# Kernel optimization log

Measured on AMD Instinct MI355X. Metric: run time of the kernel, lower is better.

## Reference

```python
import jax, jax.numpy as jnp
import numpy as np

BOX = 256      # box_size
OS = 1         # oversampling
NC = 10        # n_classes
B = 16         # batch
N = 262144     # points per example


def setup_inputs() -> dict:
    key = jax.random.key(0)
    k1, k2 = jax.random.split(key)
    # coordinates in [-0.5, 0.5) so (points+0.5)*S lies inside the grid
    points = jax.random.uniform(k1, (B, 2, N), dtype=jnp.float32, minval=-0.5, maxval=0.5)
    values = jax.random.normal(k2, (B, NC, N), dtype=jnp.float32)
    return {"points": points, "values": values}


def reference(points, values):
    S = BOX * OS
    b, nc = points.shape[0], values.shape[1]
    # [B,2,N] -> [B,N,2], scaled into pixel coords
    p = jnp.swapaxes((points + 0.5) * S, 1, 2)
    xyf = jnp.floor(p)
    r = p - xyf                       # fractional part, [B,N,2]
    xy = xyf.astype(jnp.int32)
    x, y = xy[..., 0], xy[..., 1]     # [B,N]
    rx, ry = r[..., 0], r[..., 1]

    im = jnp.zeros((b, nc, S * S), dtype=values.dtype)

    def scat(acc, idx, contrib):
        # acc [NC, S*S], idx [N], contrib [NC, N]
        return acc.at[:, idx].add(contrib)

    scat_b = jax.vmap(scat)  # over batch

    # 4-corner bilinear (CIC) deposition
    for dx in (0, 1):
        x_ = x + dx
        wx = (1 - dx) + (2 * dx - 1) * rx
        for dy in (0, 1):
            y_ = y + dy
            wy = (1 - dy) + (2 * dy - 1) * ry
            valid = (x_ >= 0) & (x_ < S) & (y_ >= 0) & (y_ < S)
            idx = jnp.where(valid, y_ * S + x_, 0)           # [B,N]
            w = jnp.where(valid, wx * wy, 0.0)               # [B,N]
            im = scat_b(im, idx, w[:, None, :] * values)     # [B,NC,S*S]

    return im.reshape(b, nc, S, S)
```

## Files before the change

kernel.cpp:

```cpp
#include <hip/hip_runtime.h>

#define S_     256
#define NC_    10
#define CHUNK  1024
#define TS     32
#define NBIN2  64
#define CAPR   4608
#define IW     33
#define IMSZ   (NC_ * IW * IW)
#define FPSCALE 262144.0f
#define FPINV   (1.0f / 262144.0f)

typedef unsigned int u32;

__device__ __forceinline__ u32 f2bf(float f) {
    u32 u = __float_as_uint(f);
    return (u + 0x7fffu + ((u >> 16) & 1u)) >> 16;
}
__device__ __forceinline__ float bf2f(u32 h) { return __uint_as_float(h << 16); }


__global__ void __launch_bounds__(256)
k_scatter(const float* __restrict__ points, const float* __restrict__ values,
          u32* __restrict__ cursor, u32* __restrict__ ovfCnt,
          u32* __restrict__ ovfBuf, uint2* __restrict__ recs, int N) {
    __shared__ u32 cnt[NBIN2];
    __shared__ u32 gOff[NBIN2];
    __shared__ unsigned char binId[CHUNK];
    __shared__ u32 lw[6][CHUNK];

    const int tid = threadIdx.x;
    const int cpb = N / CHUNK;
    const int b  = blockIdx.x / cpb;
    const int n0 = (blockIdx.x % cpb) * CHUNK;
    const float* pb = points + (size_t)b * 2 * N;
    const float* vb = values + (size_t)b * NC_ * N;
    const int nb = n0 + tid * 4;

    if (tid < NBIN2) cnt[tid] = 0;

    const float4 pxv = *(const float4*)(pb + nb);
    const float4 pyv = *(const float4*)(pb + (size_t)N + nb);
    float4 vv[NC_];
#pragma unroll
    for (int c = 0; c < NC_; ++c)
        vv[c] = *(const float4*)(vb + (size_t)c * N + nb);

    __syncthreads();

    float px4[4] = {pxv.x, pxv.y, pxv.z, pxv.w};
    float py4[4] = {pyv.x, pyv.y, pyv.z, pyv.w};
    u32 w0[4], binA[4];
#pragma unroll
    for (int k = 0; k < 4; ++k) {
        float px = (px4[k] + 0.5f) * (float)S_;
        float py = (py4[k] + 0.5f) * (float)S_;
        int xi = (int)floorf(px), yi = (int)floorf(py);
        u32 qx = __float2uint_rn((px - (float)(xi & ~31)) * 2048.0f);
        u32 qy = __float2uint_rn((py - (float)(yi & ~31)) * 2048.0f);
        qx = min(qx, 65535u); qy = min(qy, 65535u);
        w0[k] = qx | (qy << 16);
        binA[k] = (u32)(((yi >> 5) << 3) + (xi >> 5));
        atomicAdd(&cnt[binA[k]], 1u);
    }
    __syncthreads();

    if (tid < NBIN2) {
        u32 myCnt = cnt[tid];
        u32 x = myCnt;
#pragma unroll
        for (int off = 1; off < 64; off <<= 1) {
            u32 y = __shfl_up(x, off, 64);
            if (tid >= off) x += y;
        }
        u32 excl = x - myCnt;
        u32 gt = (u32)b * NBIN2 + (u32)tid;
        u32 gbase = 0;
        if (myCnt) gbase = gt * (u32)CAPR + atomicAdd(&cursor[gt], myCnt);
        gOff[tid] = gbase - excl;
        cnt[tid] = excl;
    }
    __syncthreads();

#pragma unroll
    for (int k = 0; k < 4; ++k) {
        u32 bin = binA[k];
        u32 slot = atomicAdd(&cnt[bin], 1u);
        binId[slot] = (unsigned char)bin;
#define VG(c) ((&vv[c].x)[k])
        lw[0][slot] = w0[k];
        lw[1][slot] = f2bf(VG(0)) | (f2bf(VG(1)) << 16);
        lw[2][slot] = f2bf(VG(2)) | (f2bf(VG(3)) << 16);
        lw[3][slot] = f2bf(VG(4)) | (f2bf(VG(5)) << 16);
        lw[4][slot] = f2bf(VG(6)) | (f2bf(VG(7)) << 16);
        lw[5][slot] = f2bf(VG(8)) | (f2bf(VG(9)) << 16);
#undef VG
    }
    __syncthreads();

    const u32 tb0 = (u32)b * NBIN2;
#pragma unroll
    for (int k = 0; k < 4; ++k) {
        u32 r = (u32)tid + (u32)k * 256;
        u32 bin = binId[r];
        u32 dst = gOff[bin] + r;
        u32 a0 = lw[0][r], a1 = lw[1][r], a2 = lw[2][r],
            a3 = lw[3][r], a4 = lw[4][r], a5 = lw[5][r];
        u32 rel = dst - (tb0 + bin) * (u32)CAPR;
        if (rel < (u32)CAPR) {
            size_t s3 = (size_t)dst * 3;
            recs[s3]     = make_uint2(a0, a1);
            recs[s3 + 1] = make_uint2(a2, a3);
            recs[s3 + 2] = make_uint2(a4, a5);
        } else {
            u32 oi = atomicAdd(ovfCnt, 1u);
            u32* ob = ovfBuf + (size_t)oi * 7;
            ob[0] = tb0 + bin;
            ob[1] = a0; ob[2] = a1; ob[3] = a2;
            ob[4] = a3; ob[5] = a4; ob[6] = a5;
        }
    }
}

__global__ void __launch_bounds__(256)
k_fused(const uint2* __restrict__ recs, const u32* __restrict__ cursor,
        float* __restrict__ out, float* __restrict__ borderBuf) {
    __shared__ u32 img[IMSZ];

    const int tid = threadIdx.x;
    const int g = blockIdx.x;
    const int batch = g >> 6, t = g & 63;
    const int ox = (t & 7) * TS, oy = (t >> 3) * TS;
    const u32 base = (u32)g * (u32)CAPR;
    const u32 n = min(cursor[g], (u32)CAPR);

    for (int p = tid; p < IMSZ; p += 256) img[p] = 0u;
    __syncthreads();

    for (u32 i = tid; i < n; i += 256) {
        size_t sa = (size_t)(base + i) * 3;
        uint2 a = recs[sa], b2 = recs[sa + 1], c2 = recs[sa + 2];
        u32 qx = a.x & 0xffffu, qy = a.x >> 16;
        int xi = (int)(qx >> 11), yi = (int)(qy >> 11);
        float rx = (float)(qx & 2047u) * (1.0f / 2048.0f);
        float ry = (float)(qy & 2047u) * (1.0f / 2048.0f);
        float w00 = (1.0f - rx) * (1.0f - ry) * FPSCALE;
        float w10 = rx * (1.0f - ry) * FPSCALE;
        float w01 = (1.0f - rx) * ry * FPSCALE;
        float w11 = rx * ry * FPSCALE;
        int p00 = yi * IW + xi;
        float v[NC_];
        v[0] = bf2f(a.y & 0xffffu);  v[1] = bf2f(a.y >> 16);
        v[2] = bf2f(b2.x & 0xffffu); v[3] = bf2f(b2.x >> 16);
        v[4] = bf2f(b2.y & 0xffffu); v[5] = bf2f(b2.y >> 16);
        v[6] = bf2f(c2.x & 0xffffu); v[7] = bf2f(c2.x >> 16);
        v[8] = bf2f(c2.y & 0xffffu); v[9] = bf2f(c2.y >> 16);
#pragma unroll
        for (int c = 0; c < NC_; ++c) {
            float vc = v[c];
            u32* ib = img + c * (IW * IW) + p00;
            atomicAdd(ib,          (u32)__float2int_rn(w00 * vc));
            atomicAdd(ib + 1,      (u32)__float2int_rn(w10 * vc));
            atomicAdd(ib + IW,     (u32)__float2int_rn(w01 * vc));
            atomicAdd(ib + IW + 1, (u32)__float2int_rn(w11 * vc));
        }
    }
    __syncthreads();

    for (int p = tid; p < IW * IW; p += 256) {
        int lx = p % IW, ly = p / IW;
        bool interior = (lx >= 1) & (lx <= 31) & (ly >= 1) & (ly <= 31);
        if (interior) {
            int gx = ox + lx, gy = oy + ly;
            float* ob = out + (size_t)batch * NC_ * S_ * S_ + gy * S_ + gx;
#pragma unroll
            for (int q = 0; q < NC_; ++q)
                ob[(size_t)q * S_ * S_] =
                    (float)(int)img[q * (IW * IW) + p] * FPINV;
        } else {
            float* bb = borderBuf + ((size_t)g * (IW * IW) + p) * NC_;
#pragma unroll
            for (int q = 0; q < NC_; ++q)
                bb[q] = (float)(int)img[q * (IW * IW) + p] * FPINV;
        }
    }
}

#define CLEAN_T 4096
__global__ void __launch_bounds__(256)
k_border(const float* __restrict__ borderBuf, float* __restrict__ out,
         const u32* __restrict__ ovfCnt, const u32* __restrict__ ovfBuf,
         int total) {
    int idx = blockIdx.x * 256 + threadIdx.x;
    if (idx >= total) {
        u32 oc = *ovfCnt;
        for (u32 j = (u32)(idx - total); j < oc; j += CLEAN_T) {
            const u32* ob = ovfBuf + (size_t)j * 7;
            u32 g = ob[0];
            int batch = (int)(g >> 6), t = (int)(g & 63u);
            int ox = (t & 7) * TS, oy = (t >> 3) * TS;
            u32 w0 = ob[1];
            u32 qx = w0 & 0xffffu, qy = w0 >> 16;
            int xi = ox + (int)(qx >> 11), yi = oy + (int)(qy >> 11);
            float rx = (float)(qx & 2047u) * (1.0f / 2048.0f);
            float ry = (float)(qy & 2047u) * (1.0f / 2048.0f);
            float v[NC_];
            v[0] = bf2f(ob[2] & 0xffffu); v[1] = bf2f(ob[2] >> 16);
            v[2] = bf2f(ob[3] & 0xffffu); v[3] = bf2f(ob[3] >> 16);
            v[4] = bf2f(ob[4] & 0xffffu); v[5] = bf2f(ob[4] >> 16);
            v[6] = bf2f(ob[5] & 0xffffu); v[7] = bf2f(ob[5] >> 16);
            v[8] = bf2f(ob[6] & 0xffffu); v[9] = bf2f(ob[6] >> 16);
            float* obase = out + (size_t)batch * NC_ * S_ * S_;
            for (int dx = 0; dx < 2; ++dx) {
                int x_ = xi + dx; if (x_ >= S_) continue;
                float wx = dx ? rx : (1.0f - rx);
                for (int dy = 0; dy < 2; ++dy) {
                    int y_ = yi + dy; if (y_ >= S_) continue;
                    float w = wx * (dy ? ry : (1.0f - ry));
                    for (int cc = 0; cc < NC_; ++cc)
                        atomicAdd(obase + (size_t)cc * S_ * S_ + y_ * S_ + x_,
                                  w * v[cc]);
                }
            }
        }
        return;
    }
    int b = idx / 4032;
    int j = idx - b * 4032;
    int gx, gy;
    if (j < 2048) {
        gx = (j >> 8) << 5;
        gy = j & 255;
    } else {
        int j2 = j - 2048;
        int row = j2 / 248, col = j2 - row * 248;
        gy = row << 5;
        gx = col + 1 + col / 31;
    }

    int txs[2], lxs[2], nx = 0;
    bool bx = (gx & 31) == 0, by = (gy & 31) == 0;
    if (bx) {
        if (gx > 0) { txs[nx] = (gx >> 5) - 1; lxs[nx] = 32; ++nx; }
        txs[nx] = gx >> 5; lxs[nx] = 0; ++nx;
    } else { txs[0] = gx >> 5; lxs[0] = gx & 31; nx = 1; }
    int tys[2], lys[2], ny = 0;
    if (by) {
        if (gy > 0) { tys[ny] = (gy >> 5) - 1; lys[ny] = 32; ++ny; }
        tys[ny] = gy >> 5; lys[ny] = 0; ++ny;
    } else { tys[0] = gy >> 5; lys[0] = gy & 31; ny = 1; }

    float acc[NC_];
#pragma unroll
    for (int q = 0; q < NC_; ++q) acc[q] = 0.0f;
    for (int jj = 0; jj < ny; ++jj)
        for (int ii = 0; ii < nx; ++ii) {
            int g = (b << 6) + (tys[jj] << 3) + txs[ii];
            int p = lys[jj] * IW + lxs[ii];
            const float* bb = borderBuf + ((size_t)g * (IW * IW) + p) * NC_;
#pragma unroll
            for (int q = 0; q < NC_; ++q) acc[q] += bb[q];
        }
    float* ob = out + (size_t)b * NC_ * S_ * S_ + gy * S_ + gx;
#pragma unroll
    for (int q = 0; q < NC_; ++q) ob[(size_t)q * S_ * S_] = acc[q];
}

__global__ void __launch_bounds__(256)
scatter_cic_kernel(const float* __restrict__ points,
                   const float* __restrict__ values,
                   float* __restrict__ out, int N) {
    const int n = blockIdx.x * blockDim.x + threadIdx.x;
    const int b = blockIdx.y;
    if (n >= N) return;
    const float* pb = points + (size_t)b * 2 * N;
    const float px = (pb[n] + 0.5f) * (float)S_;
    const float py = (pb[(size_t)N + n] + 0.5f) * (float)S_;
    const float xf = floorf(px), yf = floorf(py);
    const float rx = px - xf, ry = py - yf;
    const int xi = (int)xf, yi = (int)yf;
    const float* vb = values + (size_t)b * NC_ * N + n;
    float v[NC_];
#pragma unroll
    for (int c = 0; c < NC_; ++c) v[c] = vb[(size_t)c * N];
    float* ob = out + (size_t)b * NC_ * S_ * S_;
#pragma unroll
    for (int dx = 0; dx < 2; ++dx) {
        const int x_ = xi + dx;
        if (x_ < 0 || x_ >= S_) continue;
        const float wx = dx ? rx : (1.0f - rx);
#pragma unroll
        for (int dy = 0; dy < 2; ++dy) {
            const int y_ = yi + dy;
            if (y_ < 0 || y_ >= S_) continue;
            const float w = wx * (dy ? ry : (1.0f - ry));
            const int idx = y_ * S_ + x_;
#pragma unroll
            for (int c = 0; c < NC_; ++c)
                atomicAdd(ob + (size_t)c * S_ * S_ + idx, w * v[c]);
        }
    }
}

extern "C" void kernel_launch(void* const* d_in, const int* in_sizes, int n_in,
                              void* d_out, int out_size, void* d_ws, size_t ws_size,
                              hipStream_t stream) {
    const float* points = (const float*)d_in[0];
    const float* values = (const float*)d_in[1];
    float* out = (float*)d_out;

    const int B = out_size / (NC_ * S_ * S_);
    const int N = in_sizes[0] / (2 * B);

    const size_t P = (size_t)B * N;
    const int cpb = N / CHUNK;
    const int chunksTotal = B * cpb;
    const int nSlab = B * NBIN2;

    const size_t recBytes    = (size_t)nSlab * CAPR * 24;
    const size_t borderElems = (size_t)nSlab * (IW * IW) * NC_;
    const size_t ovfBytes    = P * 7 * 4;
    const size_t wsNeeded    = recBytes + (size_t)(nSlab + 1) * 4 +
                               borderElems * 4 + ovfBytes + 256;

    const bool fast = (N % CHUNK == 0) && (N >= CHUNK) && (B > 0) &&
                      (P < (1u << 31) / 2) && (ws_size >= wsNeeded);

    if (fast) {
        char* w = (char*)d_ws;
        uint2* recsA     = (uint2*)w;
        u32* cursor      = (u32*)(w + recBytes);
        u32* ovfCnt      = cursor + nSlab;
        float* borderBuf = (float*)(ovfCnt + 1);
        u32* ovfBuf      = (u32*)(borderBuf + borderElems);

        hipMemsetAsync(cursor, 0, (size_t)(nSlab + 1) * 4, stream);
        k_scatter<<<chunksTotal, 256, 0, stream>>>(points, values, cursor,
                                                   ovfCnt, ovfBuf, recsA, N);
        k_fused<<<nSlab, 256, 0, stream>>>(recsA, cursor, out, borderBuf);
        const int borderTotal = B * 4032;
        k_border<<<(borderTotal + 255) / 256 + CLEAN_T / 256, 256, 0, stream>>>(
            borderBuf, out, ovfCnt, ovfBuf, borderTotal);
    } else {
        hipMemsetAsync(d_out, 0, (size_t)out_size * sizeof(float), stream);
        dim3 block(256, 1, 1);
        dim3 grid((N + 255) / 256, B, 1);
        scatter_cic_kernel<<<grid, block, 0, stream>>>(points, values, out, N);
    }
}
```

Baseline: 352.4 us.

## Process two chunks per scatter block with early loads and prefetch records in fused

The scatter kernel now handles two 1024-point chunks per block. All loads for both chunks are issued up front through inline global_load_dwordx4, and explicit s_waitcnt vmcnt counts let the second chunk's loads stay in flight while the first chunk is binned and written. The fused kernel software-pipelines its record loop by loading the next record's three uint2 words before doing the atomics for the current one. This relies on hand-placed wait counts that the compiler cannot check, and it halves the scatter grid size and raises register pressure.

```diff
diff --git a/kernel.cpp b/kernel.cpp
--- a/kernel.cpp
+++ b/kernel.cpp
@@ -12,12 +12,16 @@
 #define FPINV   (1.0f / 262144.0f)
 
 typedef unsigned int u32;
+typedef float f32x4 __attribute__((ext_vector_type(4)));
 
 __device__ __forceinline__ u32 f2bf(float f) {
     u32 u = __float_as_uint(f);
     return (u + 0x7fffu + ((u >> 16) & 1u)) >> 16;
 }
 __device__ __forceinline__ float bf2f(u32 h) { return __uint_as_float(h << 16); }
+
+#define GLOAD4(dst, addr) \
+    asm volatile("global_load_dwordx4 %0, %1, off" : "=v"(dst) : "v"(addr))
 
 
 __global__ void __launch_bounds__(256)
@@ -30,96 +34,111 @@
     __shared__ u32 lw[6][CHUNK];
 
     const int tid = threadIdx.x;
-    const int cpb = N / CHUNK;
-    const int b  = blockIdx.x / cpb;
-    const int n0 = (blockIdx.x % cpb) * CHUNK;
+    const int ppb = N / (2 * CHUNK);
+    const int b  = blockIdx.x / ppb;
+    const int n0 = (blockIdx.x % ppb) * (2 * CHUNK);
     const float* pb = points + (size_t)b * 2 * N;
     const float* vb = values + (size_t)b * NC_ * N;
-    const int nb = n0 + tid * 4;
+    const int nA = n0 + tid * 4;
+    const int nB = nA + CHUNK;
+
+    f32x4 pxA, pyA, pxB, pyB, vA[NC_], vB[NC_];
+    GLOAD4(pxA, pb + nA);
+    GLOAD4(pyA, pb + (size_t)N + nA);
+    GLOAD4(pxB, pb + nB);
+    GLOAD4(pyB, pb + (size_t)N + nB);
+#pragma unroll
+    for (int c = 0; c < NC_; ++c) GLOAD4(vA[c], vb + (size_t)c * N + nA);
+#pragma unroll
+    for (int c = 0; c < NC_; ++c) GLOAD4(vB[c], vb + (size_t)c * N + nB);
 
     if (tid < NBIN2) cnt[tid] = 0;
-
-    const float4 pxv = *(const float4*)(pb + nb);
-    const float4 pyv = *(const float4*)(pb + (size_t)N + nb);
-    float4 vv[NC_];
-#pragma unroll
-    for (int c = 0; c < NC_; ++c)
-        vv[c] = *(const float4*)(vb + (size_t)c * N + nb);
-
-    __syncthreads();
-
-    float px4[4] = {pxv.x, pxv.y, pxv.z, pxv.w};
-    float py4[4] = {pyv.x, pyv.y, pyv.z, pyv.w};
-    u32 w0[4], binA[4];
-#pragma unroll
-    for (int k = 0; k < 4; ++k) {
-        float px = (px4[k] + 0.5f) * (float)S_;
-        float py = (py4[k] + 0.5f) * (float)S_;
-        int xi = (int)floorf(px), yi = (int)floorf(py);
-        u32 qx = __float2uint_rn((px - (float)(xi & ~31)) * 2048.0f);
-        u32 qy = __float2uint_rn((py - (float)(yi & ~31)) * 2048.0f);
-        qx = min(qx, 65535u); qy = min(qy, 65535u);
-        w0[k] = qx | (qy << 16);
-        binA[k] = (u32)(((yi >> 5) << 3) + (xi >> 5));
-        atomicAdd(&cnt[binA[k]], 1u);
-    }
-    __syncthreads();
-
-    if (tid < NBIN2) {
-        u32 myCnt = cnt[tid];
-        u32 x = myCnt;
-#pragma unroll
-        for (int off = 1; off < 64; off <<= 1) {
-            u32 y = __shfl_up(x, off, 64);
-            if (tid >= off) x += y;
-        }
-        u32 excl = x - myCnt;
-        u32 gt = (u32)b * NBIN2 + (u32)tid;
-        u32 gbase = 0;
-        if (myCnt) gbase = gt * (u32)CAPR + atomicAdd(&cursor[gt], myCnt);
-        gOff[tid] = gbase - excl;
-        cnt[tid] = excl;
-    }
-    __syncthreads();
-
-#pragma unroll
-    for (int k = 0; k < 4; ++k) {
-        u32 bin = binA[k];
-        u32 slot = atomicAdd(&cnt[bin], 1u);
-        binId[slot] = (unsigned char)bin;
-#define VG(c) ((&vv[c].x)[k])
-        lw[0][slot] = w0[k];
-        lw[1][slot] = f2bf(VG(0)) | (f2bf(VG(1)) << 16);
-        lw[2][slot] = f2bf(VG(2)) | (f2bf(VG(3)) << 16);
-        lw[3][slot] = f2bf(VG(4)) | (f2bf(VG(5)) << 16);
-        lw[4][slot] = f2bf(VG(6)) | (f2bf(VG(7)) << 16);
-        lw[5][slot] = f2bf(VG(8)) | (f2bf(VG(9)) << 16);
-#undef VG
-    }
-    __syncthreads();
-
-    const u32 tb0 = (u32)b * NBIN2;
-#pragma unroll
-    for (int k = 0; k < 4; ++k) {
-        u32 r = (u32)tid + (u32)k * 256;
-        u32 bin = binId[r];
-        u32 dst = gOff[bin] + r;
-        u32 a0 = lw[0][r], a1 = lw[1][r], a2 = lw[2][r],
-            a3 = lw[3][r], a4 = lw[4][r], a5 = lw[5][r];
-        u32 rel = dst - (tb0 + bin) * (u32)CAPR;
-        if (rel < (u32)CAPR) {
-            size_t s3 = (size_t)dst * 3;
-            recs[s3]     = make_uint2(a0, a1);
-            recs[s3 + 1] = make_uint2(a2, a3);
-            recs[s3 + 2] = make_uint2(a4, a5);
-        } else {
-            u32 oi = atomicAdd(ovfCnt, 1u);
-            u32* ob = ovfBuf + (size_t)oi * 7;
-            ob[0] = tb0 + bin;
-            ob[1] = a0; ob[2] = a1; ob[3] = a2;
-            ob[4] = a3; ob[5] = a4; ob[6] = a5;
-        }
-    }
+    __syncthreads();
+
+    auto process = [&](const f32x4& pxv, const f32x4& pyv,
+                       const f32x4 (&vv)[NC_], bool firstChunk) {
+        u32 w0[4], binA[4];
+#pragma unroll
+        for (int k = 0; k < 4; ++k) {
+            float px = (pxv[k] + 0.5f) * (float)S_;
+            float py = (pyv[k] + 0.5f) * (float)S_;
+            int xi = (int)floorf(px), yi = (int)floorf(py);
+            u32 qx = __float2uint_rn((px - (float)(xi & ~31)) * 2048.0f);
+            u32 qy = __float2uint_rn((py - (float)(yi & ~31)) * 2048.0f);
+            qx = min(qx, 65535u); qy = min(qy, 65535u);
+            w0[k] = qx | (qy << 16);
+            binA[k] = (u32)(((yi >> 5) << 3) + (xi >> 5));
+            atomicAdd(&cnt[binA[k]], 1u);
+        }
+        __syncthreads();
+
+        if (tid < NBIN2) {
+            u32 myCnt = cnt[tid];
+            u32 x = myCnt;
+#pragma unroll
+            for (int off = 1; off < 64; off <<= 1) {
+                u32 y = __shfl_up(x, off, 64);
+                if (tid >= off) x += y;
+            }
+            u32 excl = x - myCnt;
+            u32 gt = (u32)b * NBIN2 + (u32)tid;
+            u32 gbase = 0;
+            if (myCnt) gbase = gt * (u32)CAPR + atomicAdd(&cursor[gt], myCnt);
+            gOff[tid] = gbase - excl;
+            cnt[tid] = excl;
+        }
+        __syncthreads();
+
+        if (firstChunk) asm volatile("s_waitcnt vmcnt(10)");
+        else            asm volatile("s_waitcnt vmcnt(0)");
+        __builtin_amdgcn_sched_barrier(0);
+
+#pragma unroll
+        for (int k = 0; k < 4; ++k) {
+            u32 bin = binA[k];
+            u32 slot = atomicAdd(&cnt[bin], 1u);
+            binId[slot] = (unsigned char)bin;
+            lw[0][slot] = w0[k];
+            lw[1][slot] = f2bf(vv[0][k]) | (f2bf(vv[1][k]) << 16);
+            lw[2][slot] = f2bf(vv[2][k]) | (f2bf(vv[3][k]) << 16);
+            lw[3][slot] = f2bf(vv[4][k]) | (f2bf(vv[5][k]) << 16);
+            lw[4][slot] = f2bf(vv[6][k]) | (f2bf(vv[7][k]) << 16);
+            lw[5][slot] = f2bf(vv[8][k]) | (f2bf(vv[9][k]) << 16);
+        }
+        __syncthreads();
+
+        const u32 tb0 = (u32)b * NBIN2;
+#pragma unroll
+        for (int k = 0; k < 4; ++k) {
+            u32 r = (u32)tid + (u32)k * 256;
+            u32 bin = binId[r];
+            u32 dst = gOff[bin] + r;
+            u32 a0 = lw[0][r], a1 = lw[1][r], a2 = lw[2][r],
+                a3 = lw[3][r], a4 = lw[4][r], a5 = lw[5][r];
+            u32 rel = dst - (tb0 + bin) * (u32)CAPR;
+            if (rel < (u32)CAPR) {
+                size_t s3 = (size_t)dst * 3;
+                recs[s3]     = make_uint2(a0, a1);
+                recs[s3 + 1] = make_uint2(a2, a3);
+                recs[s3 + 2] = make_uint2(a4, a5);
+            } else {
+                u32 oi = atomicAdd(ovfCnt, 1u);
+                u32* ob = ovfBuf + (size_t)oi * 7;
+                ob[0] = tb0 + bin;
+                ob[1] = a0; ob[2] = a1; ob[3] = a2;
+                ob[4] = a3; ob[5] = a4; ob[6] = a5;
+            }
+        }
+    };
+
+    asm volatile("s_waitcnt vmcnt(20)");
+    __builtin_amdgcn_sched_barrier(0);
+    process(pxA, pyA, vA, true);
+
+    __syncthreads();
+    if (tid < NBIN2) cnt[tid] = 0;
+    __syncthreads();
+    process(pxB, pyB, vB, false);
 }
 
 __global__ void __launch_bounds__(256)
@@ -137,10 +156,20 @@
     for (int p = tid; p < IMSZ; p += 256) img[p] = 0u;
     __syncthreads();
 
-    for (u32 i = tid; i < n; i += 256) {
-        size_t sa = (size_t)(base + i) * 3;
-        uint2 a = recs[sa], b2 = recs[sa + 1], c2 = recs[sa + 2];
-        u32 qx = a.x & 0xffffu, qy = a.x >> 16;
+    u32 i = tid;
+    uint2 a0, a1, a2;
+    if (i < n) {
+        const uint2* rp = recs + (size_t)(base + i) * 3;
+        a0 = rp[0]; a1 = rp[1]; a2 = rp[2];
+    }
+    while (i < n) {
+        u32 j = i + 256;
+        uint2 b0, b1, b2;
+        if (j < n) {
+            const uint2* rp = recs + (size_t)(base + j) * 3;
+            b0 = rp[0]; b1 = rp[1]; b2 = rp[2];
+        }
+        u32 qx = a0.x & 0xffffu, qy = a0.x >> 16;
         int xi = (int)(qx >> 11), yi = (int)(qy >> 11);
         float rx = (float)(qx & 2047u) * (1.0f / 2048.0f);
         float ry = (float)(qy & 2047u) * (1.0f / 2048.0f);
@@ -150,11 +179,15 @@
         float w11 = rx * ry * FPSCALE;
         int p00 = yi * IW + xi;
         float v[NC_];
-        v[0] = bf2f(a.y & 0xffffu);  v[1] = bf2f(a.y >> 16);
-        v[2] = bf2f(b2.x & 0xffffu); v[3] = bf2f(b2.x >> 16);
-        v[4] = bf2f(b2.y & 0xffffu); v[5] = bf2f(b2.y >> 16);
-        v[6] = bf2f(c2.x & 0xffffu); v[7] = bf2f(c2.x >> 16);
-        v[8] = bf2f(c2.y & 0xffffu); v[9] = bf2f(c2.y >> 16);
+        v[0] = bf2f(a1.x & 0xffffu); v[1] = bf2f(a1.x >> 16);
+        v[2] = bf2f(a1.y & 0xffffu); v[3] = bf2f(a1.y >> 16);
+        v[4] = bf2f(a2.x & 0xffffu); v[5] = bf2f(a2.x >> 16);
+        v[6] = bf2f(a2.y & 0xffffu); v[7] = bf2f(a2.y >> 16);
+        v[0] = bf2f(a0.y & 0xffffu); v[1] = bf2f(a0.y >> 16);
+        v[2] = bf2f(a1.x & 0xffffu); v[3] = bf2f(a1.x >> 16);
+        v[4] = bf2f(a1.y & 0xffffu); v[5] = bf2f(a1.y >> 16);
+        v[6] = bf2f(a2.x & 0xffffu); v[7] = bf2f(a2.x >> 16);
+        v[8] = bf2f(a2.y & 0xffffu); v[9] = bf2f(a2.y >> 16);
 #pragma unroll
         for (int c = 0; c < NC_; ++c) {
             float vc = v[c];
@@ -164,6 +197,8 @@
             atomicAdd(ib + IW,     (u32)__float2int_rn(w01 * vc));
             atomicAdd(ib + IW + 1, (u32)__float2int_rn(w11 * vc));
         }
+        a0 = b0; a1 = b1; a2 = b2;
+        i = j;
     }
     __syncthreads();
 
@@ -313,8 +348,7 @@
     const int N = in_sizes[0] / (2 * B);
 
     const size_t P = (size_t)B * N;
-    const int cpb = N / CHUNK;
-    const int chunksTotal = B * cpb;
+    const int pairsTotal = B * (N / (2 * CHUNK));
     const int nSlab = B * NBIN2;
 
     const size_t recBytes    = (size_t)nSlab * CAPR * 24;
@@ -323,7 +357,7 @@
     const size_t wsNeeded    = recBytes + (size_t)(nSlab + 1) * 4 +
                                borderElems * 4 + ovfBytes + 256;
 
-    const bool fast = (N % CHUNK == 0) && (N >= CHUNK) && (B > 0) &&
+    const bool fast = (N % (2 * CHUNK) == 0) && (N >= 2 * CHUNK) && (B > 0) &&
                       (P < (1u << 31) / 2) && (ws_size >= wsNeeded);
 
     if (fast) {
@@ -335,8 +369,8 @@
         u32* ovfBuf      = (u32*)(borderBuf + borderElems);
 
         hipMemsetAsync(cursor, 0, (size_t)(nSlab + 1) * 4, stream);
-        k_scatter<<<chunksTotal, 256, 0, stream>>>(points, values, cursor,
-                                                   ovfCnt, ovfBuf, recsA, N);
+        k_scatter<<<pairsTotal, 256, 0, stream>>>(points, values, cursor,
+                                                  ovfCnt, ovfBuf, recsA, N);
         k_fused<<<nSlab, 256, 0, stream>>>(recsA, cursor, out, borderBuf);
         const int borderTotal = B * 4032;
         k_border<<<(borderTotal + 255) / 256 + CLEAN_T / 256, 256, 0, stream>>>(
```

After: 347.6 us. About the same (-1.4%).

## Store records as three planar arrays and prefetch next record in fused kernel

Applied to the files above, without the earlier changes.

Changes the record buffer from interleaved 24-byte records to three planes of 8-byte uint2s, so each load and store across a wavefront is contiguous and coalesced. The fused kernel also software-pipelines its loop, issuing loads for the next record before running the atomics for the current one, to hide global memory latency. The fast path is now limited to B==16 because the plane stride is a compile-time constant.

```diff
diff --git a/kernel.cpp b/kernel.cpp
--- a/kernel.cpp
+++ b/kernel.cpp
@@ -6,6 +6,8 @@
 #define TS     32
 #define NBIN2  64
 #define CAPR   4608
+#define NSLAB  1024
+#define PSTR   ((size_t)NSLAB * CAPR)
 #define IW     33
 #define IMSZ   (NC_ * IW * IW)
 #define FPSCALE 262144.0f
@@ -108,10 +110,9 @@
             a3 = lw[3][r], a4 = lw[4][r], a5 = lw[5][r];
         u32 rel = dst - (tb0 + bin) * (u32)CAPR;
         if (rel < (u32)CAPR) {
-            size_t s3 = (size_t)dst * 3;
-            recs[s3]     = make_uint2(a0, a1);
-            recs[s3 + 1] = make_uint2(a2, a3);
-            recs[s3 + 2] = make_uint2(a4, a5);
+            recs[dst]            = make_uint2(a0, a1);
+            recs[PSTR + dst]     = make_uint2(a2, a3);
+            recs[2 * PSTR + dst] = make_uint2(a4, a5);
         } else {
             u32 oi = atomicAdd(ovfCnt, 1u);
             u32* ob = ovfBuf + (size_t)oi * 7;
@@ -137,10 +138,22 @@
     for (int p = tid; p < IMSZ; p += 256) img[p] = 0u;
     __syncthreads();
 
-    for (u32 i = tid; i < n; i += 256) {
-        size_t sa = (size_t)(base + i) * 3;
-        uint2 a = recs[sa], b2 = recs[sa + 1], c2 = recs[sa + 2];
-        u32 qx = a.x & 0xffffu, qy = a.x >> 16;
+    u32 i = tid;
+    uint2 a0, a1, a2;
+    if (i < n) {
+        a0 = recs[base + i];
+        a1 = recs[PSTR + base + i];
+        a2 = recs[2 * PSTR + base + i];
+    }
+    while (i < n) {
+        u32 j = i + 256;
+        uint2 b0, b1, b2;
+        if (j < n) {
+            b0 = recs[base + j];
+            b1 = recs[PSTR + base + j];
+            b2 = recs[2 * PSTR + base + j];
+        }
+        u32 qx = a0.x & 0xffffu, qy = a0.x >> 16;
         int xi = (int)(qx >> 11), yi = (int)(qy >> 11);
         float rx = (float)(qx & 2047u) * (1.0f / 2048.0f);
         float ry = (float)(qy & 2047u) * (1.0f / 2048.0f);
@@ -150,11 +163,11 @@
         float w11 = rx * ry * FPSCALE;
         int p00 = yi * IW + xi;
         float v[NC_];
-        v[0] = bf2f(a.y & 0xffffu);  v[1] = bf2f(a.y >> 16);
-        v[2] = bf2f(b2.x & 0xffffu); v[3] = bf2f(b2.x >> 16);
-        v[4] = bf2f(b2.y & 0xffffu); v[5] = bf2f(b2.y >> 16);
-        v[6] = bf2f(c2.x & 0xffffu); v[7] = bf2f(c2.x >> 16);
-        v[8] = bf2f(c2.y & 0xffffu); v[9] = bf2f(c2.y >> 16);
+        v[0] = bf2f(a0.y & 0xffffu); v[1] = bf2f(a0.y >> 16);
+        v[2] = bf2f(a1.x & 0xffffu); v[3] = bf2f(a1.x >> 16);
+        v[4] = bf2f(a1.y & 0xffffu); v[5] = bf2f(a1.y >> 16);
+        v[6] = bf2f(a2.x & 0xffffu); v[7] = bf2f(a2.x >> 16);
+        v[8] = bf2f(a2.y & 0xffffu); v[9] = bf2f(a2.y >> 16);
 #pragma unroll
         for (int c = 0; c < NC_; ++c) {
             float vc = v[c];
@@ -164,6 +177,8 @@
             atomicAdd(ib + IW,     (u32)__float2int_rn(w01 * vc));
             atomicAdd(ib + IW + 1, (u32)__float2int_rn(w11 * vc));
         }
+        a0 = b0; a1 = b1; a2 = b2;
+        i = j;
     }
     __syncthreads();
 
@@ -317,14 +332,15 @@
     const int chunksTotal = B * cpb;
     const int nSlab = B * NBIN2;
 
-    const size_t recBytes    = (size_t)nSlab * CAPR * 24;
+    const size_t recBytes    = 3 * PSTR * 8;
     const size_t borderElems = (size_t)nSlab * (IW * IW) * NC_;
     const size_t ovfBytes    = P * 7 * 4;
     const size_t wsNeeded    = recBytes + (size_t)(nSlab + 1) * 4 +
                                borderElems * 4 + ovfBytes + 256;
 
-    const bool fast = (N % CHUNK == 0) && (N >= CHUNK) && (B > 0) &&
-                      (P < (1u << 31) / 2) && (ws_size >= wsNeeded);
+    const bool fast = (N % CHUNK == 0) && (N >= CHUNK) && (B == 16) &&
+                      (nSlab == NSLAB) && (P < (1u << 31) / 2) &&
+                      (ws_size >= wsNeeded);
 
     if (fast) {
         char* w = (char*)d_ws;
```

New measurement: 355.6 us. Within noise of the previous version (+0.9%).
